# Kernel optimization log

Hardware: AMD Instinct MI355X
Metric: run time of the kernel (lower is better)

## Reference

```python
import jax, jax.numpy as jnp
import numpy as np

LN_EPS = 1e-5

def setup_inputs() -> dict:
    key = jax.random.key(0)
    ks = jax.random.split(key, 9)
    B, N, D, E, H = 1, 50000, 128, 800000, 8
    s = 1.0 / np.sqrt(D)
    x = jax.random.normal(ks[0], (B, N, D), jnp.float32)
    edge_index = jax.random.randint(ks[1], (2, E), 0, N, dtype=jnp.int64)
    edge_weights = jax.random.uniform(ks[2], (E,), jnp.float32)
    Wq = jax.random.normal(ks[3], (D, D), jnp.float32) * s
    Wk = jax.random.normal(ks[4], (D, D), jnp.float32) * s
    Wv = jax.random.normal(ks[5], (D, D), jnp.float32) * s
    We = jax.random.normal(ks[6], (H, 1), jnp.float32)  # edge_encoder: Linear(1, H, bias=False)
    Wo = jax.random.normal(ks[7], (D, D), jnp.float32) * s
    gamma = jnp.ones((D,), jnp.float32)
    beta = jnp.zeros((D,), jnp.float32)
    return {"x": x, "edge_index": edge_index, "edge_weights": edge_weights,
            "Wq": Wq, "Wk": Wk, "Wv": Wv, "We": We, "Wo": Wo,
            "gamma": gamma, "beta": beta}


def reference(x, edge_index, edge_weights, Wq, Wk, Wv, We, Wo, gamma, beta):
    B, N, D = x.shape
    H = We.shape[0]
    d = D // H
    scale = 1.0 / np.sqrt(d)

    # QKV projections -> [B, N, H, d]
    Q = (x @ Wq.T).reshape(B, N, H, d)
    K = (x @ Wk.T).reshape(B, N, H, d)
    V = (x @ Wv.T).reshape(B, N, H, d)

    src, dst = edge_index[0], edge_index[1]

    # Edge-indexed gathers: [B, E, H, d]
    Qe = Q[:, src]
    Ke = K[:, dst]
    Ve = V[:, dst]

    # Per-edge scores [B, E, H] + edge bias (Linear(1,H) on edge_weights)
    scores = jnp.einsum('behd,behd->beh', Qe, Ke) * scale
    scores = scores + (edge_weights[:, None] * We[None, :, 0])[None]  # [1,E,H]

    # Segment (scatter) softmax over src neighborhoods, segment axis first: [E, B, H]
    s = jnp.moveaxis(scores, 1, 0)
    m = jax.ops.segment_max(s, src, num_segments=N)          # [N, B, H]
    e = jnp.exp(s - m[src])
    denom = jax.ops.segment_sum(e, src, num_segments=N)      # [N, B, H]
    attn = e / denom[src]                                    # [E, B, H]

    # Weighted scatter-add aggregation: [N, B, H, d]
    wV = attn[..., None] * jnp.moveaxis(Ve, 1, 0)
    agg = jax.ops.segment_sum(wV, src, num_segments=N)

    attn_out = jnp.moveaxis(agg, 0, 1).reshape(B, N, D)
    out = attn_out @ Wo.T

    # Residual + LayerNorm
    y = x + out
    mu = y.mean(-1, keepdims=True)
    var = ((y - mu) ** 2).mean(-1, keepdims=True)
    return (y - mu) / jnp.sqrt(var + LN_EPS) * gamma + beta
```

## Files before the change

### kernel.cpp

```cpp
#include <hip/hip_runtime.h>
#include <hip/hip_bf16.h>
#include <math.h>


#define CAP 64

typedef __attribute__((ext_vector_type(8))) short short8;
typedef __attribute__((ext_vector_type(4))) float f32x4;

static __device__ __forceinline__ ushort f2bf(float f) {
  unsigned u = __float_as_uint(f);
  u += 0x7fff + ((u >> 16) & 1);
  return (ushort)(u >> 16);
}
static __device__ __forceinline__ float bflo(unsigned u) {
  return __uint_as_float(u << 16);
}
static __device__ __forceinline__ float bfhi(unsigned u) {
  return __uint_as_float(u & 0xffff0000u);
}

__global__ __launch_bounds__(256) void prep_kernel(
    const float* __restrict__ Wq, const float* __restrict__ Wk,
    const float* __restrict__ Wv, const float* __restrict__ Wo,
    ushort* __restrict__ Wb) {
  int tid = blockIdx.x * 256 + threadIdx.x;
  if (tid < 16384) {
    int i = tid * 4;
    const float* src = (i < 16384) ? Wq : (i < 32768) ? Wk : (i < 49152) ? Wv : Wo;
    int off = i & 16383;
    float4 v = *(const float4*)(src + off);
    *(ushort4*)(Wb + i) = make_ushort4(f2bf(v.x), f2bf(v.y), f2bf(v.z), f2bf(v.w));
  }
}

__global__ __launch_bounds__(256) void qkv_histfill_kernel(
    const float* __restrict__ x, const ushort* __restrict__ Wb,
    float* __restrict__ Qf, ushort* __restrict__ KVb,
    const int* __restrict__ ei, const float* __restrict__ ew,
    int* __restrict__ cnt, unsigned* __restrict__ recs,
    int N, int E, int QB) {
  if ((int)blockIdx.x >= QB) {
    int sb = (int)blockIdx.x - QB;
    int p  = sb & 3;
    int k  = sb >> 2;
    int lo = (int)((long)N * p >> 2);
    int hi = (int)((long)N * (p + 1) >> 2);
    int e0 = k * 2048 + (int)threadIdx.x * 8;
#pragma unroll
    for (int i = 0; i < 8; i++) {
      int e = e0 + i;
      if (e < E) {
        int s = ei[e];
        if (s >= lo && s < hi) {
          int r = atomicAdd(&cnt[s], 1);
          if (r < CAP) {
            unsigned pk = ((unsigned)ei[E + e] << 15) | ((unsigned)f2bf(ew[e]) & 0x7fffu);
            recs[((size_t)s << 6) + r] = pk;
          }
        }
      }
    }
    return;
  }
  int bid = (int)blockIdx.x;
  int m = bid % 3, t = bid / 3;
  int w = threadIdx.x >> 6, l = threadIdx.x & 63;
  int n0 = t * 256 + w * 64;
  int lr = l & 15, lg = l >> 4;

  short8 a[4][4];
#pragma unroll
  for (int rt = 0; rt < 4; rt++) {
    int arow = n0 + rt * 16 + lr;
    if (arow < N) {
      const float* xrow = x + (size_t)arow * 128 + 8 * lg;
      float4 x0[4], x1[4];
#pragma unroll
      for (int ks = 0; ks < 4; ks++) {
        x0[ks] = *(const float4*)(xrow + 32 * ks);
        x1[ks] = *(const float4*)(xrow + 32 * ks + 4);
      }
#pragma unroll
      for (int ks = 0; ks < 4; ks++) {
        short8 tt;
        tt[0] = f2bf(x0[ks].x); tt[1] = f2bf(x0[ks].y); tt[2] = f2bf(x0[ks].z); tt[3] = f2bf(x0[ks].w);
        tt[4] = f2bf(x1[ks].x); tt[5] = f2bf(x1[ks].y); tt[6] = f2bf(x1[ks].z); tt[7] = f2bf(x1[ks].w);
        a[rt][ks] = tt;
      }
    } else {
#pragma unroll
      for (int ks = 0; ks < 4; ks++) a[rt][ks] = (short8){0,0,0,0,0,0,0,0};
    }
  }

  const ushort* Wm = Wb + m * 16384;
#pragma unroll
  for (int ctp = 0; ctp < 4; ctp++) {
    short8 b[2][4];
#pragma unroll
    for (int ci = 0; ci < 2; ci++) {
      const ushort* wrow = Wm + (size_t)((ctp * 2 + ci) * 16 + lr) * 128 + 8 * lg;
#pragma unroll
      for (int ks = 0; ks < 4; ks++) b[ci][ks] = *(const short8*)(wrow + 32 * ks);
    }
#pragma unroll
    for (int rt = 0; rt < 4; rt++) {
#pragma unroll
      for (int ci = 0; ci < 2; ci++) {
        f32x4 acc = {0.f, 0.f, 0.f, 0.f};
#pragma unroll
        for (int ks = 0; ks < 4; ks++)
          acc = __builtin_amdgcn_mfma_f32_16x16x32_bf16(a[rt][ks], b[ci][ks], acc, 0, 0, 0);
        int c = (ctp * 2 + ci) * 16 + lr;
#pragma unroll
        for (int r = 0; r < 4; r++) {
          int row = n0 + rt * 16 + 4 * lg + r;
          if (row < N) {
            if (m == 0)      Qf[(size_t)row * 128 + c] = acc[r];
            else if (m == 1) KVb[(size_t)row * 256 + c] = f2bf(acc[r]);
            else             KVb[(size_t)row * 256 + 128 + c] = f2bf(acc[r]);
          }
        }
      }
    }
  }
}

__global__ __launch_bounds__(256) void edge_attn_kernel(
    const float* __restrict__ Qf, const ushort* __restrict__ KVb,
    const unsigned* __restrict__ recs, const float* __restrict__ We,
    const int* __restrict__ cnt, ushort* __restrict__ AGGb, int N) {
  int wv = threadIdx.x >> 6, l = threadIdx.x & 63;
  int n = blockIdx.x * 4 + wv;
  if (n >= N) return;
  int u = l >> 3, h = l & 7;
  int deg = min(cnt[n], CAP);
  ushort* op = AGGb + (size_t)n * 128 + (h << 4);

  if (deg <= 0) {
    if (u == 0) {
      *(uint4*)(op + 0) = make_uint4(0, 0, 0, 0);
      *(uint4*)(op + 8) = make_uint4(0, 0, 0, 0);
    }
    return;
  }

  const unsigned* rb = recs + ((size_t)n << 6);
  unsigned myrec = rb[min(l, deg - 1)];

  float q[16];
  const float* qp = Qf + (size_t)n * 128 + (h << 4);
  *(float4*)(q + 0)  = *(const float4*)(qp + 0);
  *(float4*)(q + 4)  = *(const float4*)(qp + 4);
  *(float4*)(q + 8)  = *(const float4*)(qp + 8);
  *(float4*)(q + 12) = *(const float4*)(qp + 12);
  float weh = We[h];

  float m = -INFINITY, de = 0.f;
  float acc[16];
#pragma unroll
  for (int d = 0; d < 16; d++) acc[d] = 0.f;

  for (int base = 0; base < deg; base += 8) {
    int idx = base + u;
    unsigned rec = __shfl(myrec, idx);
    const ushort* kv = KVb + (((rec >> 15) << 8) + (h << 4));
    uint4 k0 = *(const uint4*)kv;
    uint4 k1 = *(const uint4*)(kv + 8);
    uint4 v0 = *(const uint4*)(kv + 128);
    uint4 v1 = *(const uint4*)(kv + 136);

    float s;
    s  = q[0]  * bflo(k0.x) + q[1]  * bfhi(k0.x);
    s += q[2]  * bflo(k0.y) + q[3]  * bfhi(k0.y);
    s += q[4]  * bflo(k0.z) + q[5]  * bfhi(k0.z);
    s += q[6]  * bflo(k0.w) + q[7]  * bfhi(k0.w);
    s += q[8]  * bflo(k1.x) + q[9]  * bfhi(k1.x);
    s += q[10] * bflo(k1.y) + q[11] * bfhi(k1.y);
    s += q[12] * bflo(k1.z) + q[13] * bfhi(k1.z);
    s += q[14] * bflo(k1.w) + q[15] * bfhi(k1.w);
    s = s * 0.25f + __uint_as_float((rec & 0x7fffu) << 16) * weh;
    if (idx >= deg) s = -INFINITY;

    float p;
    if (s > m + 8.f) {
      float c = __expf(m - s);
      de *= c;
#pragma unroll
      for (int d = 0; d < 16; d++) acc[d] *= c;
      m = s;
      p = 1.f;
    } else {
      p = __expf(s - m);
    }
    de += p;
    acc[0]  += p * bflo(v0.x); acc[1]  += p * bfhi(v0.x);
    acc[2]  += p * bflo(v0.y); acc[3]  += p * bfhi(v0.y);
    acc[4]  += p * bflo(v0.z); acc[5]  += p * bfhi(v0.z);
    acc[6]  += p * bflo(v0.w); acc[7]  += p * bfhi(v0.w);
    acc[8]  += p * bflo(v1.x); acc[9]  += p * bfhi(v1.x);
    acc[10] += p * bflo(v1.y); acc[11] += p * bfhi(v1.y);
    acc[12] += p * bflo(v1.z); acc[13] += p * bfhi(v1.z);
    acc[14] += p * bflo(v1.w); acc[15] += p * bfhi(v1.w);
  }

  bool live = (m > -INFINITY);
  if (!live) {
    de = 0.f;
#pragma unroll
    for (int d = 0; d < 16; d++) acc[d] = 0.f;
  }
  float M = m;
  M = fmaxf(M, __shfl_xor(M, 8));
  M = fmaxf(M, __shfl_xor(M, 16));
  M = fmaxf(M, __shfl_xor(M, 32));
  float c = live ? __expf(m - M) : 0.f;
  de *= c;
#pragma unroll
  for (int d = 0; d < 16; d++) acc[d] *= c;
  de += __shfl_xor(de, 8); de += __shfl_xor(de, 16); de += __shfl_xor(de, 32);
#pragma unroll
  for (int d = 0; d < 16; d++) {
    acc[d] += __shfl_xor(acc[d], 8);
    acc[d] += __shfl_xor(acc[d], 16);
    acc[d] += __shfl_xor(acc[d], 32);
  }

  if (u == 0) {
    float inv = (de > 0.f) ? 1.0f / de : 0.f;
    unsigned o[8];
#pragma unroll
    for (int j = 0; j < 8; j++) {
      ushort lo = f2bf(acc[2 * j] * inv);
      ushort hi = f2bf(acc[2 * j + 1] * inv);
      o[j] = (unsigned)lo | ((unsigned)hi << 16);
    }
    *(uint4*)(op + 0) = make_uint4(o[0], o[1], o[2], o[3]);
    *(uint4*)(op + 8) = make_uint4(o[4], o[5], o[6], o[7]);
  }
}

__global__ __launch_bounds__(256) void wo_ln_kernel(
    const ushort* __restrict__ AGGb, const ushort* __restrict__ Wob,
    const float* __restrict__ x, const float* __restrict__ gamma,
    const float* __restrict__ beta, float* __restrict__ out, int N) {
  int w = threadIdx.x >> 6, l = threadIdx.x & 63;
  int n0 = blockIdx.x * 128 + w * 32;
  int lr = l & 15, lg = l >> 4;

  short8 a[2][4];
#pragma unroll
  for (int rt = 0; rt < 2; rt++) {
    int arow = n0 + rt * 16 + lr;
    if (arow < N) {
      const ushort* ap = AGGb + (size_t)arow * 128 + 8 * lg;
#pragma unroll
      for (int ks = 0; ks < 4; ks++) a[rt][ks] = *(const short8*)(ap + 32 * ks);
    } else {
#pragma unroll
      for (int ks = 0; ks < 4; ks++) a[rt][ks] = (short8){0,0,0,0,0,0,0,0};
    }
  }

  f32x4 acc[2][8];
#pragma unroll
  for (int ctp = 0; ctp < 4; ctp++) {
    short8 b[2][4];
#pragma unroll
    for (int ci = 0; ci < 2; ci++) {
      const ushort* wrow = Wob + (size_t)((ctp * 2 + ci) * 16 + lr) * 128 + 8 * lg;
#pragma unroll
      for (int ks = 0; ks < 4; ks++) b[ci][ks] = *(const short8*)(wrow + 32 * ks);
    }
#pragma unroll
    for (int rt = 0; rt < 2; rt++)
#pragma unroll
      for (int ci = 0; ci < 2; ci++) {
        int ct = ctp * 2 + ci;
        acc[rt][ct] = (f32x4){0.f, 0.f, 0.f, 0.f};
#pragma unroll
        for (int ks = 0; ks < 4; ks++)
          acc[rt][ct] = __builtin_amdgcn_mfma_f32_16x16x32_bf16(a[rt][ks], b[ci][ks], acc[rt][ct], 0, 0, 0);
      }
  }
  float g[8], bt[8];
#pragma unroll
  for (int ct = 0; ct < 8; ct++) { g[ct] = gamma[ct * 16 + lr]; bt[ct] = beta[ct * 16 + lr]; }

#pragma unroll
  for (int rt = 0; rt < 2; rt++) {
#pragma unroll
    for (int r = 0; r < 4; r++) {
      int row = n0 + rt * 16 + 4 * lg + r;
      bool ok = row < N;
      float v[8], s = 0.f, s2 = 0.f;
#pragma unroll
      for (int ct = 0; ct < 8; ct++) {
        float xv = ok ? x[(size_t)row * 128 + ct * 16 + lr] : 0.f;
        v[ct] = acc[rt][ct][r] + xv;
        s += v[ct]; s2 += v[ct] * v[ct];
      }
#pragma unroll
      for (int d = 1; d < 16; d <<= 1) { s += __shfl_xor(s, d); s2 += __shfl_xor(s2, d); }
      float mu = s * (1.f / 128.f);
      float var = s2 * (1.f / 128.f) - mu * mu;
      float rs = rsqrtf(var + 1e-5f);
      if (ok) {
#pragma unroll
        for (int ct = 0; ct < 8; ct++)
          out[(size_t)row * 128 + ct * 16 + lr] = (v[ct] - mu) * rs * g[ct] + bt[ct];
      }
    }
  }
}

extern "C" void kernel_launch(void* const* d_in, const int* in_sizes, int n_in,
                              void* d_out, int out_size, void* d_ws, size_t ws_size,
                              hipStream_t stream) {
  const float* x     = (const float*)d_in[0];
  const int*   ei    = (const int*)d_in[1];
  const float* ew    = (const float*)d_in[2];
  const float* Wq    = (const float*)d_in[3];
  const float* Wk    = (const float*)d_in[4];
  const float* Wv    = (const float*)d_in[5];
  const float* We    = (const float*)d_in[6];
  const float* Wo    = (const float*)d_in[7];
  const float* gamma = (const float*)d_in[8];
  const float* beta  = (const float*)d_in[9];

  int N = in_sizes[0] / 128;
  int E = in_sizes[1] / 2;
  int Npad = (N + 255) & ~255;
  int QB = 3 * (Npad / 256);
  int SB = 4 * ((E + 2047) / 2048);

  char* ws = (char*)d_ws;
  ushort* Wb   = (ushort*)ws; ws += 4 * 16384 * 2;
  float*  Qf   = (float*)ws;  ws += (size_t)Npad * 128 * 4;
  ushort* KVb  = (ushort*)ws; ws += (size_t)Npad * 256 * 2;
  ushort* AGGb = (ushort*)ws; ws += (size_t)Npad * 128 * 2;
  int* cnt  = (int*)ws; ws += (size_t)N * 4;
  unsigned* recs = (unsigned*)ws; ws += (size_t)N * CAP * 4;
  ushort* Wob = Wb + 3 * 16384;

  hipMemsetAsync(cnt, 0, (size_t)N * 4, stream);

  prep_kernel<<<64, 256, 0, stream>>>(Wq, Wk, Wv, Wo, Wb);

  qkv_histfill_kernel<<<QB + SB, 256, 0, stream>>>(x, Wb, Qf, KVb, ei, ew, cnt, recs, N, E, QB);

  edge_attn_kernel<<<(N + 3) / 4, 256, 0, stream>>>(Qf, KVb, recs, We, cnt, AGGb, N);

  wo_ln_kernel<<<Npad / 128, 256, 0, stream>>>(AGGb, Wob, x, gamma, beta, (float*)d_out, N);
}
```

Baseline: 150.6 us.

## Replace direct per-node edge scatter with two-pass binned counting sort

Edge bucketing becomes two passes. First, each block bins 2048 edges into 256 coarse source-node bins using shared-memory staging, then appends them to global per-bin arrays. A separate kernel then scatters each bin into per-node slots with atomics. The aim is locality: global atomics and record writes for nearby nodes land close together, instead of being scattered across all nodes, and the four-way redundant reads of the edge list go away. The cost is an extra kernel launch, a serial prefix scan by one thread per block, and a fixed per-bin capacity of 4096; edges beyond that are silently dropped, and with about 3125 expected edges per bin overflow is unlikely but not guaranteed.

```diff
diff --git a/kernel.cpp b/kernel.cpp
--- a/kernel.cpp
+++ b/kernel.cpp
@@ -3,10 +3,13 @@
 #include <math.h>
 
 
-#define CAP 64
+#define CAP  64
+#define NBIN 256
+#define CAPB 4096
 
 typedef __attribute__((ext_vector_type(8))) short short8;
 typedef __attribute__((ext_vector_type(4))) float f32x4;
+typedef __attribute__((ext_vector_type(4))) int i32x4;
 
 static __device__ __forceinline__ ushort f2bf(float f) {
   unsigned u = __float_as_uint(f);
@@ -34,35 +37,70 @@
   }
 }
 
-__global__ __launch_bounds__(256) void qkv_histfill_kernel(
+__global__ __launch_bounds__(256) void qkv_binA_kernel(
     const float* __restrict__ x, const ushort* __restrict__ Wb,
     float* __restrict__ Qf, ushort* __restrict__ KVb,
     const int* __restrict__ ei, const float* __restrict__ ew,
-    int* __restrict__ cnt, unsigned* __restrict__ recs,
+    int* __restrict__ binCnt, uint2* __restrict__ binArr,
     int N, int E, int QB) {
+  __shared__ int  lcnt[NBIN];
+  __shared__ int  loff[NBIN];
+  __shared__ int  lpos[NBIN];
+  __shared__ int  gbase[NBIN];
+  __shared__ uint2 stage[2048];
+
   if ((int)blockIdx.x >= QB) {
     int sb = (int)blockIdx.x - QB;
-    int p  = sb & 3;
-    int k  = sb >> 2;
-    int lo = (int)((long)N * p >> 2);
-    int hi = (int)((long)N * (p + 1) >> 2);
-    int e0 = k * 2048 + (int)threadIdx.x * 8;
+    int t  = threadIdx.x;
+    int e0 = sb * 2048 + t * 8;
+    int nblk = min(2048, E - sb * 2048);
+    if (nblk < 0) nblk = 0;
+
+    lcnt[t] = 0;
+    __syncthreads();
+
+    int ss[8], dd[8]; float ww[8]; int bn[8];
+    bool val[8];
 #pragma unroll
     for (int i = 0; i < 8; i++) {
       int e = e0 + i;
-      if (e < E) {
-        int s = ei[e];
-        if (s >= lo && s < hi) {
-          int r = atomicAdd(&cnt[s], 1);
-          if (r < CAP) {
-            unsigned pk = ((unsigned)ei[E + e] << 15) | ((unsigned)f2bf(ew[e]) & 0x7fffu);
-            recs[((size_t)s << 6) + r] = pk;
-          }
-        }
-      }
+      val[i] = e < E;
+      if (val[i]) { ss[i] = ei[e]; dd[i] = ei[E + e]; ww[i] = ew[e]; }
+      else        { ss[i] = 0; dd[i] = 0; ww[i] = 0.f; }
+      bn[i] = (int)((long)ss[i] * NBIN / N);
+      if (val[i]) atomicAdd(&lcnt[bn[i]], 1);
+    }
+    __syncthreads();
+
+    if (t == 0) {
+      int a = 0;
+      for (int b = 0; b < NBIN; b++) { int c = lcnt[b]; loff[b] = a; lpos[b] = a; a += c; }
+    }
+    __syncthreads();
+
+#pragma unroll
+    for (int i = 0; i < 8; i++) {
+      if (val[i]) {
+        int p = atomicAdd(&lpos[bn[i]], 1);
+        stage[p] = make_uint2(((unsigned)ss[i] << 15) | ((unsigned)f2bf(ww[i]) & 0x7fffu),
+                              (unsigned)dd[i]);
+      }
+    }
+    __syncthreads();
+
+    gbase[t] = (lcnt[t] > 0) ? atomicAdd(&binCnt[t], lcnt[t]) : 0;
+    __syncthreads();
+
+    for (int i = t; i < nblk; i += 256) {
+      uint2 rec = stage[i];
+      int s = (int)(rec.x >> 15);
+      int b = (int)((long)s * NBIN / N);
+      int pos = gbase[b] + (i - loff[b]);
+      if (pos < CAPB) binArr[(size_t)b * CAPB + pos] = rec;
     }
     return;
   }
+
   int bid = (int)blockIdx.x;
   int m = bid % 3, t = bid / 3;
   int w = threadIdx.x >> 6, l = threadIdx.x & 63;
@@ -124,6 +162,20 @@
         }
       }
     }
+  }
+}
+
+__global__ __launch_bounds__(256) void passB_kernel(
+    const int* __restrict__ binCnt, const uint2* __restrict__ binArr,
+    int* __restrict__ cnt, unsigned* __restrict__ recs, int N, int E) {
+  int b = blockIdx.x;
+  int nb = min(binCnt[b], CAPB);
+  const uint2* arr = binArr + (size_t)b * CAPB;
+  for (int i = threadIdx.x; i < nb; i += 256) {
+    uint2 rec = arr[i];
+    int s = (int)(rec.x >> 15);
+    int r = atomicAdd(&cnt[s], 1);
+    if (r < CAP) recs[((size_t)s << 6) + r] = (rec.y << 15) | (rec.x & 0x7fffu);
   }
 }
 
@@ -333,7 +385,7 @@
   int E = in_sizes[1] / 2;
   int Npad = (N + 255) & ~255;
   int QB = 3 * (Npad / 256);
-  int SB = 4 * ((E + 2047) / 2048);
+  int BA = (E + 2047) / 2048;
 
   char* ws = (char*)d_ws;
   ushort* Wb   = (ushort*)ws; ws += 4 * 16384 * 2;
@@ -342,13 +394,18 @@
   ushort* AGGb = (ushort*)ws; ws += (size_t)Npad * 128 * 2;
   int* cnt  = (int*)ws; ws += (size_t)N * 4;
   unsigned* recs = (unsigned*)ws; ws += (size_t)N * CAP * 4;
+  int* binCnt = (int*)ws; ws += (size_t)NBIN * 4;
+  uint2* binArr = (uint2*)ws; ws += (size_t)NBIN * CAPB * 8;
   ushort* Wob = Wb + 3 * 16384;
 
   hipMemsetAsync(cnt, 0, (size_t)N * 4, stream);
+  hipMemsetAsync(binCnt, 0, (size_t)NBIN * 4, stream);
 
   prep_kernel<<<64, 256, 0, stream>>>(Wq, Wk, Wv, Wo, Wb);
 
-  qkv_histfill_kernel<<<QB + SB, 256, 0, stream>>>(x, Wb, Qf, KVb, ei, ew, cnt, recs, N, E, QB);
+  qkv_binA_kernel<<<QB + BA, 256, 0, stream>>>(x, Wb, Qf, KVb, ei, ew, binCnt, binArr, N, E, QB);
+
+  passB_kernel<<<NBIN, 256, 0, stream>>>(binCnt, binArr, cnt, recs, N, E);
 
   edge_attn_kernel<<<(N + 3) / 4, 256, 0, stream>>>(Qf, KVb, recs, We, cnt, AGGb, N);
 
```

Result: faster. 146.3 us (-2.8%).
